# Kernel tuning notes

Hardware: AMD Instinct MI355X
Metric: run time of the kernel (lower is better)

Reference implementation:

```python
import jax, jax.numpy as jnp
import numpy as np

N_DRUG = 572
EMB = 256
K_NB = 128
N_TAIL = 100000
N_REL = 200
N_EDGE = 4576
BN_EPS = 1e-5


def setup_inputs() -> dict:
    key = jax.random.key(0)
    ks = jax.random.split(key, 12)
    return {
        "drug_name": jnp.arange(N_DRUG, dtype=jnp.int64 if jax.config.jax_enable_x64 else jnp.int32),
        "adj_tail": jax.random.randint(ks[0], (N_DRUG, K_NB), 0, N_TAIL),
        "adj_relation": jax.random.randint(ks[1], (N_DRUG, K_NB), 0, N_REL),
        "nb_src": jax.random.randint(ks[2], (N_EDGE,), 0, N_DRUG),
        "nb_dst": jax.random.randint(ks[3], (N_EDGE,), 0, N_DRUG),
        "epoch": 2,
        # learned parameters
        "drug_table": jax.random.normal(ks[4], (N_DRUG, EMB), dtype=jnp.float32),
        "rela_table": jax.random.normal(ks[5], (N_REL, EMB), dtype=jnp.float32),
        "ent_table": jax.random.normal(ks[6], (N_TAIL, EMB), dtype=jnp.float32),
        "lin_W": jax.random.normal(ks[7], (2 * EMB, EMB), dtype=jnp.float32) * (1.0 / np.sqrt(2 * EMB)),
        "lin_b": jnp.zeros((EMB,), dtype=jnp.float32),
        "bn_gamma": jnp.ones((EMB,), dtype=jnp.float32),
        "bn_beta": jnp.zeros((EMB,), dtype=jnp.float32),
    }


def reference(drug_name, adj_tail, adj_relation, nb_src, nb_dst, epoch,
              drug_table, rela_table, ent_table, lin_W, lin_b, bn_gamma, bn_beta):
    # --- embedding gathers ---
    d = drug_table[drug_name]          # [N, E]
    r = rela_table[adj_relation]       # [N, K, E]
    e = ent_table[adj_tail]            # [N, K, E]

    # --- attention over sampled neighbors (KGNN-style: score = <drug, relation>) ---
    scores = jnp.einsum('ne,nke->nk', d, r)              # [N, K]
    alpha = jax.nn.softmax(scores, axis=1)               # softmax over neighbors
    attended = jnp.einsum('nk,nke->ne', alpha, e)        # [N, E]

    # --- Linear(2E -> E) + ReLU + BatchNorm1d (training-mode batch stats) ---
    x = jnp.concatenate([attended, d], axis=1)           # [N, 2E]
    h = jax.nn.relu(x @ lin_W + lin_b)                   # [N, E]
    mean = jnp.mean(h, axis=0)
    var = jnp.mean((h - mean) ** 2, axis=0)              # biased var, as in torch BN
    drug_f = (h - mean) * jax.lax.rsqrt(var + BN_EPS) * bn_gamma + bn_beta

    # --- invariant-adjacency segment-average scatter update (epoch > 1) ---
    if epoch > 1:
        nb_sum = jax.ops.segment_sum(drug_f[nb_src], nb_dst, num_segments=N_DRUG)   # [N, E]
        cnt = jax.ops.segment_sum(jnp.ones_like(nb_dst, dtype=drug_f.dtype), nb_dst,
                                  num_segments=N_DRUG)                               # [N]
        nb_avg = nb_sum / jnp.maximum(cnt, 1.0)[:, None]
        drug_f = jnp.where((cnt > 0)[:, None], (nb_avg + drug_f) * 0.5, drug_f)
    return drug_f
```

## Files before the change

### kernel.cpp

```cpp
#include <hip/hip_runtime.h>

#define N_DRUG 572
#define EMB    256
#define K_NB   128
#define N_EDGE 4576
#define BN_EPS 1e-5f

__global__ __launch_bounds__(256) void fused_attn_lin(
    const int* __restrict__ drug_name,
    const int* __restrict__ adj_tail,
    const int* __restrict__ adj_relation,
    const float* __restrict__ drug_table,
    const float* __restrict__ rela_table,
    const float* __restrict__ ent_table,
    const float* __restrict__ lin_W,
    const float* __restrict__ lin_b,
    float* __restrict__ h,
    float* __restrict__ s1,
    float* __restrict__ s2)
{
    __shared__ float xs[2 * EMB];
    __shared__ float sc[K_NB];
    __shared__ int   tails[K_NB];
    __shared__ int   rels[K_NB];
    __shared__ float part[4][EMB];
    __shared__ float wred[2];

    const int b    = blockIdx.x;
    const int tid  = threadIdx.x;
    const int lane = tid & 63;
    const int wv   = tid >> 6;

    const int didx = drug_name[b];
    xs[EMB + tid] = drug_table[(size_t)didx * EMB + tid];
    if (tid < K_NB) {
        tails[tid] = adj_tail[b * K_NB + tid];
        rels[tid]  = adj_relation[b * K_NB + tid];
    }
    __syncthreads();

    const float4 dv = ((const float4*)(xs + EMB))[lane];
    for (int k = wv; k < K_NB; k += 4) {
        const float4 rv = ((const float4*)(rela_table + (size_t)rels[k] * EMB))[lane];
        float p = dv.x * rv.x + dv.y * rv.y + dv.z * rv.z + dv.w * rv.w;
        #pragma unroll
        for (int off = 32; off > 0; off >>= 1)
            p += __shfl_xor(p, off, 64);
        if (lane == 0) sc[k] = p;
    }
    __syncthreads();

    float pv = 0.f;
    if (tid < K_NB) {
        float m = sc[tid];
        #pragma unroll
        for (int off = 32; off > 0; off >>= 1)
            m = fmaxf(m, __shfl_xor(m, off, 64));
        if (lane == 0) wred[wv] = m;
    }
    __syncthreads();
    if (tid < K_NB) {
        const float m = fmaxf(wred[0], wred[1]);
        pv = __expf(sc[tid] - m);
        float s = pv;
        #pragma unroll
        for (int off = 32; off > 0; off >>= 1)
            s += __shfl_xor(s, off, 64);
        if (lane == 0) wred[wv] = s;
    }
    __syncthreads();
    if (tid < K_NB) {
        const float tot = wred[0] + wred[1];
        sc[tid] = pv / tot;
    }
    __syncthreads();

    float4 acc = make_float4(0.f, 0.f, 0.f, 0.f);
    #pragma unroll 8
    for (int kk = 0; kk < 32; ++kk) {
        const int k = wv * 32 + kk;
        const float a = sc[k];
        const float4 ev = ((const float4*)(ent_table + (size_t)tails[k] * EMB))[lane];
        acc.x = fmaf(a, ev.x, acc.x);
        acc.y = fmaf(a, ev.y, acc.y);
        acc.z = fmaf(a, ev.z, acc.z);
        acc.w = fmaf(a, ev.w, acc.w);
    }
    ((float4*)part[wv])[lane] = acc;
    __syncthreads();
    xs[tid] = part[0][tid] + part[1][tid] + part[2][tid] + part[3][tid];
    __syncthreads();

    float accL = 0.f;
    #pragma unroll 8
    for (int i = 0; i < 2 * EMB; ++i)
        accL = fmaf(xs[i], lin_W[(size_t)i * EMB + tid], accL);

    const float v = fmaxf(accL + lin_b[tid], 0.f);
    h[(size_t)b * EMB + tid] = v;
    atomicAdd(&s1[tid], v);
    atomicAdd(&s2[tid], v * v);
}

#define EPB 8
__global__ __launch_bounds__(256) void scatter_bn(
    const int* __restrict__ nb_src, const int* __restrict__ nb_dst,
    const int* __restrict__ epoch,
    const float* __restrict__ h,
    const float* __restrict__ s1, const float* __restrict__ s2,
    const float* __restrict__ gamma, const float* __restrict__ beta,
    float* __restrict__ nb_sum,
    float* __restrict__ cnt)
{
    if (*epoch <= 1) return;
    const int tid = threadIdx.x;
    const float invN  = 1.0f / (float)N_DRUG;
    const float mean  = s1[tid] * invN;
    const float var   = s2[tid] * invN - mean * mean;
    const float scale = gamma[tid] * rsqrtf(var + BN_EPS);
    const float bet   = beta[tid];

    const int e0 = blockIdx.x * EPB;
    const int e1 = min(e0 + EPB, N_EDGE);
    for (int e = e0; e < e1; ++e) {
        const int s = nb_src[e];
        const int d = nb_dst[e];
        const float f = (h[(size_t)s * EMB + tid] - mean) * scale + bet;
        atomicAdd(&nb_sum[(size_t)d * EMB + tid], f);
        if (tid == 0) atomicAdd(&cnt[d], 1.0f);
    }
}

__global__ __launch_bounds__(256) void combine_bn(
    const float* __restrict__ h,
    const float* __restrict__ s1, const float* __restrict__ s2,
    const float* __restrict__ gamma, const float* __restrict__ beta,
    const float* __restrict__ nb_sum,
    const float* __restrict__ cnt,
    const int* __restrict__ epoch,
    float* __restrict__ out)
{
    const int b   = blockIdx.x;
    const int tid = threadIdx.x;
    const size_t idx = (size_t)b * EMB + tid;
    const float invN  = 1.0f / (float)N_DRUG;
    const float mean  = s1[tid] * invN;
    const float var   = s2[tid] * invN - mean * mean;
    const float scale = gamma[tid] * rsqrtf(var + BN_EPS);
    float f = (h[idx] - mean) * scale + beta[tid];
    if (*epoch > 1) {
        const float c = cnt[b];
        if (c > 0.f) f = (nb_sum[idx] / c + f) * 0.5f;
    }
    out[idx] = f;
}

extern "C" void kernel_launch(void* const* d_in, const int* in_sizes, int n_in,
                              void* d_out, int out_size, void* d_ws, size_t ws_size,
                              hipStream_t stream) {
    const int*   drug_name    = (const int*)d_in[0];
    const int*   adj_tail     = (const int*)d_in[1];
    const int*   adj_relation = (const int*)d_in[2];
    const int*   nb_src       = (const int*)d_in[3];
    const int*   nb_dst       = (const int*)d_in[4];
    const int*   epoch        = (const int*)d_in[5];
    const float* drug_table   = (const float*)d_in[6];
    const float* rela_table   = (const float*)d_in[7];
    const float* ent_table    = (const float*)d_in[8];
    const float* lin_W        = (const float*)d_in[9];
    const float* lin_b        = (const float*)d_in[10];
    const float* bn_gamma     = (const float*)d_in[11];
    const float* bn_beta      = (const float*)d_in[12];
    float* out = (float*)d_out;

    float* ws = (float*)d_ws;
    float* h      = ws;
    float* s1     = h + N_DRUG * EMB;
    float* s2     = s1 + EMB;
    float* cnt    = s2 + EMB;
    float* nb_sum = cnt + N_DRUG;
    const size_t zero_bytes = (size_t)(EMB + EMB + N_DRUG + N_DRUG * EMB) * sizeof(float);

    hipMemsetAsync(s1, 0, zero_bytes, stream);

    fused_attn_lin<<<N_DRUG, 256, 0, stream>>>(drug_name, adj_tail, adj_relation,
                                               drug_table, rela_table, ent_table,
                                               lin_W, lin_b, h, s1, s2);

    scatter_bn<<<(N_EDGE + EPB - 1) / EPB, 256, 0, stream>>>(nb_src, nb_dst, epoch,
                                                             h, s1, s2, bn_gamma, bn_beta,
                                                             nb_sum, cnt);

    combine_bn<<<N_DRUG, 256, 0, stream>>>(h, s1, s2, bn_gamma, bn_beta,
                                           nb_sum, cnt, epoch, out);
}
```

Before: 233.8 us.

## Split fused attention kernel into scores, chunked gather, and split-K linear kernels

```diff
diff --git a/kernel.cpp b/kernel.cpp
--- a/kernel.cpp
+++ b/kernel.cpp
@@ -6,24 +6,15 @@
 #define N_EDGE 4576
 #define BN_EPS 1e-5f
 
-__global__ __launch_bounds__(256) void fused_attn_lin(
+__global__ __launch_bounds__(256) void scores_kernel(
     const int* __restrict__ drug_name,
-    const int* __restrict__ adj_tail,
     const int* __restrict__ adj_relation,
     const float* __restrict__ drug_table,
     const float* __restrict__ rela_table,
-    const float* __restrict__ ent_table,
-    const float* __restrict__ lin_W,
-    const float* __restrict__ lin_b,
-    float* __restrict__ h,
-    float* __restrict__ s1,
-    float* __restrict__ s2)
-{
-    __shared__ float xs[2 * EMB];
+    float* __restrict__ alphas)
+{
+    __shared__ float ld[EMB];
     __shared__ float sc[K_NB];
-    __shared__ int   tails[K_NB];
-    __shared__ int   rels[K_NB];
-    __shared__ float part[4][EMB];
     __shared__ float wred[2];
 
     const int b    = blockIdx.x;
@@ -31,17 +22,13 @@
     const int lane = tid & 63;
     const int wv   = tid >> 6;
 
-    const int didx = drug_name[b];
-    xs[EMB + tid] = drug_table[(size_t)didx * EMB + tid];
-    if (tid < K_NB) {
-        tails[tid] = adj_tail[b * K_NB + tid];
-        rels[tid]  = adj_relation[b * K_NB + tid];
-    }
-    __syncthreads();
-
-    const float4 dv = ((const float4*)(xs + EMB))[lane];
+    ld[tid] = drug_table[(size_t)drug_name[b] * EMB + tid];
+    __syncthreads();
+
+    const float4 dv = ((const float4*)ld)[lane];
     for (int k = wv; k < K_NB; k += 4) {
-        const float4 rv = ((const float4*)(rela_table + (size_t)rels[k] * EMB))[lane];
+        const int rel = adj_relation[b * K_NB + k];
+        const float4 rv = ((const float4*)(rela_table + (size_t)rel * EMB))[lane];
         float p = dv.x * rv.x + dv.y * rv.y + dv.z * rv.z + dv.w * rv.w;
         #pragma unroll
         for (int off = 32; off > 0; off >>= 1)
@@ -71,16 +58,33 @@
     __syncthreads();
     if (tid < K_NB) {
         const float tot = wred[0] + wred[1];
-        sc[tid] = pv / tot;
-    }
-    __syncthreads();
-
+        alphas[(size_t)b * K_NB + tid] = pv / tot;
+    }
+}
+
+#define NCHUNK 4
+#define CK (K_NB / NCHUNK)
+__global__ __launch_bounds__(256) void gather_kernel(
+    const int* __restrict__ adj_tail,
+    const float* __restrict__ alphas,
+    const float* __restrict__ ent_table,
+    float* __restrict__ att)
+{
+    __shared__ float part[4][EMB];
+
+    const int b    = blockIdx.x / NCHUNK;
+    const int c    = blockIdx.x % NCHUNK;
+    const int tid  = threadIdx.x;
+    const int lane = tid & 63;
+    const int wv   = tid >> 6;
+
+    const int base = b * K_NB + c * CK + wv * 8;
     float4 acc = make_float4(0.f, 0.f, 0.f, 0.f);
-    #pragma unroll 8
-    for (int kk = 0; kk < 32; ++kk) {
-        const int k = wv * 32 + kk;
-        const float a = sc[k];
-        const float4 ev = ((const float4*)(ent_table + (size_t)tails[k] * EMB))[lane];
+    #pragma unroll
+    for (int j = 0; j < 8; ++j) {
+        const float a = alphas[base + j];
+        const int   t = adj_tail[base + j];
+        const float4 ev = ((const float4*)(ent_table + (size_t)t * EMB))[lane];
         acc.x = fmaf(a, ev.x, acc.x);
         acc.y = fmaf(a, ev.y, acc.y);
         acc.z = fmaf(a, ev.z, acc.z);
@@ -88,18 +92,47 @@
     }
     ((float4*)part[wv])[lane] = acc;
     __syncthreads();
-    xs[tid] = part[0][tid] + part[1][tid] + part[2][tid] + part[3][tid];
-    __syncthreads();
-
-    float accL = 0.f;
+    const float v = part[0][tid] + part[1][tid] + part[2][tid] + part[3][tid];
+    atomicAdd(&att[(size_t)b * EMB + tid], v);
+}
+
+__global__ __launch_bounds__(512) void linear_kernel(
+    const int* __restrict__ drug_name,
+    const float* __restrict__ att,
+    const float* __restrict__ drug_table,
+    const float* __restrict__ lin_W,
+    const float* __restrict__ lin_b,
+    float* __restrict__ h,
+    float* __restrict__ s1,
+    float* __restrict__ s2)
+{
+    __shared__ float xs[2 * EMB];
+    __shared__ float part[2][EMB];
+
+    const int b   = blockIdx.x;
+    const int tid = threadIdx.x;
+
+    if (tid < EMB) xs[tid] = att[(size_t)b * EMB + tid];
+    else           xs[tid] = drug_table[(size_t)drug_name[b] * EMB + (tid - EMB)];
+    __syncthreads();
+
+    const int col  = tid & (EMB - 1);
+    const int half = tid >> 8;
+    const float* wp = lin_W + (size_t)(half * EMB) * EMB + col;
+    const float* xp = xs + half * EMB;
+    float acc = 0.f;
     #pragma unroll 8
-    for (int i = 0; i < 2 * EMB; ++i)
-        accL = fmaf(xs[i], lin_W[(size_t)i * EMB + tid], accL);
-
-    const float v = fmaxf(accL + lin_b[tid], 0.f);
-    h[(size_t)b * EMB + tid] = v;
-    atomicAdd(&s1[tid], v);
-    atomicAdd(&s2[tid], v * v);
+    for (int i = 0; i < EMB; ++i)
+        acc = fmaf(xp[i], wp[(size_t)i * EMB], acc);
+    part[half][col] = acc;
+    __syncthreads();
+
+    if (tid < EMB) {
+        const float v = fmaxf(part[0][tid] + part[1][tid] + lin_b[tid], 0.f);
+        h[(size_t)b * EMB + tid] = v;
+        atomicAdd(&s1[tid], v);
+        atomicAdd(&s2[tid], v * v);
+    }
 }
 
 #define EPB 8
@@ -179,13 +212,21 @@
     float* s2     = s1 + EMB;
     float* cnt    = s2 + EMB;
     float* nb_sum = cnt + N_DRUG;
-    const size_t zero_bytes = (size_t)(EMB + EMB + N_DRUG + N_DRUG * EMB) * sizeof(float);
+    float* att    = nb_sum + N_DRUG * EMB;
+    float* alphas = att + N_DRUG * EMB;
+    const size_t zero_bytes =
+        (size_t)(EMB + EMB + N_DRUG + 2 * N_DRUG * EMB) * sizeof(float);
 
     hipMemsetAsync(s1, 0, zero_bytes, stream);
 
-    fused_attn_lin<<<N_DRUG, 256, 0, stream>>>(drug_name, adj_tail, adj_relation,
-                                               drug_table, rela_table, ent_table,
-                                               lin_W, lin_b, h, s1, s2);
+    scores_kernel<<<N_DRUG, 256, 0, stream>>>(drug_name, adj_relation,
+                                              drug_table, rela_table, alphas);
+
+    gather_kernel<<<N_DRUG * NCHUNK, 256, 0, stream>>>(adj_tail, alphas,
+                                                       ent_table, att);
+
+    linear_kernel<<<N_DRUG, 512, 0, stream>>>(drug_name, att, drug_table,
+                                              lin_W, lin_b, h, s1, s2);
 
     scatter_bn<<<(N_EDGE + EPB - 1) / EPB, 256, 0, stream>>>(nb_src, nb_dst, epoch,
                                                              h, s1, s2, bn_gamma, bn_beta,
```

After: 232.1 us. About the same (-0.7%).
